# Kernel tuning notes

Measured on AMD Instinct MI355X. Metric: run time of the kernel, lower is better.

Reference implementation:

```python
import jax, jax.numpy as jnp
import numpy as np

H = 64  # hidden_dimension
F = 8   # number_of_input_features
P = 64  # prediction_length
B = 1024
T = 512


def _lstm_cell(x, h, c, Wih, Whh, bih, bhh):
    # PyTorch gate order: input, forget, cell(g), output
    gates = x @ Wih.T + h @ Whh.T + (bih + bhh)  # [B, 4H]
    i, f, g, o = jnp.split(gates, 4, axis=-1)
    c_new = jax.nn.sigmoid(f) * c + jax.nn.sigmoid(i) * jnp.tanh(g)
    h_new = jax.nn.sigmoid(o) * jnp.tanh(c_new)
    return h_new, c_new


def setup_inputs() -> dict:
    key = jax.random.key(0)
    ks = jax.random.split(key, 11)
    s = 1.0 / np.sqrt(H)
    u = lambda k, shape: jax.random.uniform(k, shape, jnp.float32, -s, s)
    return {
        "input_sequence": jax.random.normal(ks[0], (B, T, F), jnp.float32),
        "enc_Wih": u(ks[1], (4 * H, F)),
        "enc_Whh": u(ks[2], (4 * H, H)),
        "enc_bih": u(ks[3], (4 * H,)),
        "enc_bhh": u(ks[4], (4 * H,)),
        "dec_Wih": u(ks[5], (4 * H, F)),
        "dec_Whh": u(ks[6], (4 * H, H)),
        "dec_bih": u(ks[7], (4 * H,)),
        "dec_bhh": u(ks[8], (4 * H,)),
        "fc_W": u(ks[9], (F, H)),
        "fc_b": u(ks[10], (F,)),
    }


def reference(input_sequence, enc_Wih, enc_Whh, enc_bih, enc_bhh,
              dec_Wih, dec_Whh, dec_bih, dec_bhh, fc_W, fc_b):
    Bn = input_sequence.shape[0]
    h0 = jnp.zeros((Bn, H), input_sequence.dtype)
    c0 = jnp.zeros((Bn, H), input_sequence.dtype)

    # ---- Encoder: scan over time ----
    xs = jnp.swapaxes(input_sequence, 0, 1)  # [T, B, F]

    def enc_step(carry, x_t):
        h, c = carry
        h, c = _lstm_cell(x_t, h, c, enc_Wih, enc_Whh, enc_bih, enc_bhh)
        return (h, c), None

    (h, c), _ = jax.lax.scan(enc_step, (h0, c0), xs)

    x_last = input_sequence[:, -1, :]  # [B, F]

    def dec_step(carry, _):
        h, c, x = carry
        h, c = _lstm_cell(x, h, c, dec_Wih, dec_Whh, dec_bih, dec_bhh)
        pred = h @ fc_W.T + fc_b  # [B, F]
        return (h, c, pred), pred

    _, preds = jax.lax.scan(dec_step, (h, c, x_last), None, length=P)
    return jnp.swapaxes(preds, 0, 1)  # [B, P, F]
```

## Files before the change

### kernel.cpp

```cpp
#include <hip/hip_runtime.h>


#define Hh 64
#define Ff 8
#define Tt 512
#define Pp 64
#define BATCH 1024
#define MB 4
#define NBLK (BATCH / MB)
#define ROWS 72
#define ABUF (16 * ROWS + 64)
#define XSTRIDE 32

typedef __attribute__((ext_vector_type(8))) _Float16 half8;
typedef __attribute__((ext_vector_type(4))) _Float16 half4;
typedef __attribute__((ext_vector_type(4))) float f32x4;

#define LOG2E  1.44269504088896340736f
#define K2LOG2 2.88538008177792681472f

__device__ __forceinline__ float sig_pre(float a) {
    return __builtin_amdgcn_rcpf(1.f + __builtin_amdgcn_exp2f(-a));
}
__device__ __forceinline__ float tanh_pre(float a) {
    return 1.f - 2.f * __builtin_amdgcn_rcpf(1.f + __builtin_amdgcn_exp2f(a));
}
__device__ __forceinline__ int arow_base(int m) { return m * ROWS + (m & 3) * 16; }

__device__ __forceinline__ void load_wfrags(
    const float* __restrict__ Whh, const float* __restrict__ Wih,
    int wv, int q, int col, half8 w0[4], half8 w1[4], half8 wx[4])
{
    #pragma unroll
    for (int Tg = 0; Tg < 4; ++Tg) {
        int g = Tg * 64 + wv * 16 + col;
        float sc = (Tg == 2) ? K2LOG2 : LOG2E;
        const float* r0 = Whh + g * 64 + q * 8;
        #pragma unroll
        for (int j = 0; j < 8; ++j) {
            w0[Tg][j] = (_Float16)(r0[j] * sc);
            w1[Tg][j] = (_Float16)(r0[32 + j] * sc);
            wx[Tg][j] = (q == 0) ? (_Float16)(Wih[g * 8 + j] * sc) : (_Float16)0.f;
        }
    }
}

__device__ __forceinline__ void pchain(half8 ax, const half8 wx[4],
                                       const f32x4 biasv[4], f32x4 P[4])
{
    P[2] = __builtin_amdgcn_mfma_f32_16x16x32_f16(ax, wx[2], biasv[2], 0, 0, 0);
    P[0] = __builtin_amdgcn_mfma_f32_16x16x32_f16(ax, wx[0], biasv[0], 0, 0, 0);
    P[1] = __builtin_amdgcn_mfma_f32_16x16x32_f16(ax, wx[1], biasv[1], 0, 0, 0);
    P[3] = __builtin_amdgcn_mfma_f32_16x16x32_f16(ax, wx[3], biasv[3], 0, 0, 0);
}

__device__ __forceinline__ float qcell(half8 a0, half8 a1,
    const half8 w0[4], const half8 w1[4], const f32x4 P[4], float& cS)
{
    f32x4 Qg = __builtin_amdgcn_mfma_f32_16x16x32_f16(a0, w0[2], P[2], 0, 0, 0);
    f32x4 Qi = __builtin_amdgcn_mfma_f32_16x16x32_f16(a0, w0[0], P[0], 0, 0, 0);
    f32x4 Qf = __builtin_amdgcn_mfma_f32_16x16x32_f16(a0, w0[1], P[1], 0, 0, 0);
    f32x4 Qo = __builtin_amdgcn_mfma_f32_16x16x32_f16(a0, w0[3], P[3], 0, 0, 0);
    Qg = __builtin_amdgcn_mfma_f32_16x16x32_f16(a1, w1[2], Qg, 0, 0, 0);
    Qi = __builtin_amdgcn_mfma_f32_16x16x32_f16(a1, w1[0], Qi, 0, 0, 0);
    Qf = __builtin_amdgcn_mfma_f32_16x16x32_f16(a1, w1[1], Qf, 0, 0, 0);
    Qo = __builtin_amdgcn_mfma_f32_16x16x32_f16(a1, w1[3], Qo, 0, 0, 0);
    float tg = tanh_pre(Qg[0]);
    float si = sig_pre(Qi[0]);
    float sf = sig_pre(Qf[0]);
    float so = sig_pre(Qo[0]);
    cS = sf * cS + (si * tg) * K2LOG2;
    return so * tanh_pre(cS);
}

__global__ __launch_bounds__(256, 1)
void seq2seq_v8(const float* __restrict__ x_seq,
                const float* __restrict__ eWih, const float* __restrict__ eWhh,
                const float* __restrict__ ebih, const float* __restrict__ ebhh,
                const float* __restrict__ dWih, const float* __restrict__ dWhh,
                const float* __restrict__ dbih, const float* __restrict__ dbhh,
                const float* __restrict__ fcW,  const float* __restrict__ fcb,
                float* __restrict__ out)
{
    __shared__ __align__(16) _Float16 xs[(Tt + 4) * XSTRIDE];
    __shared__ __align__(16) _Float16 A0[ABUF];
    __shared__ __align__(16) _Float16 A1[ABUF];
    __shared__ float fcWT[Hh * 9 + 8];
    __shared__ float sfcb[Ff];
    __shared__ __align__(16) _Float16 xdec[MB * Ff];

    const int tid  = threadIdx.x;
    const int wv   = tid >> 6;
    const int lane = tid & 63;
    const int q    = lane >> 4;
    const int col  = lane & 15;
    const int u    = wv * 16 + col;
    const int b0   = blockIdx.x * MB;

    half8 w0[4], w1[4], wx[4];
    load_wfrags(eWhh, eWih, wv, q, col, w0, w1, wx);
    f32x4 biasv[4];
    #pragma unroll
    for (int Tg = 0; Tg < 4; ++Tg) {
        int g = Tg * 64 + u;
        float sc = (Tg == 2) ? K2LOG2 : LOG2E;
        float bv = (ebih[g] + ebhh[g]) * sc;
        biasv[Tg] = (f32x4){bv, bv, bv, bv};
    }

    { int* Z0 = (int*)A0; int* Z1 = (int*)A1;
      for (int i = tid; i < ABUF / 2; i += 256) { Z0[i] = 0; Z1[i] = 0; } }
    for (int i = tid; i < Ff * Hh; i += 256) { int f = i >> 6, uu = i & 63; fcWT[uu * 9 + f] = fcW[i]; }
    if (tid < Ff) sfcb[tid] = fcb[tid];
    if (tid < 64) ((int*)xs)[Tt * 16 + tid] = 0;
    for (int i = tid; i < MB * Tt * 2; i += 256) {
        int b   = i >> 10;
        int rem = i & 1023;
        int t   = rem >> 1;
        int f4  = (rem & 1) * 4;
        const float* src = x_seq + ((size_t)(b0 + b) * Tt + t) * Ff + f4;
        half4 s = { (_Float16)src[0], (_Float16)src[1], (_Float16)src[2], (_Float16)src[3] };
        *(half4*)(&xs[t * XSTRIDE + b * 8 + f4]) = s;
    }
    __syncthreads();

    const _Float16* arA = A0 + arow_base(col) + q * 8;
    const _Float16* arB = A1 + arow_base(col) + q * 8;
    _Float16* hwA = A0 + 4 * q * ROWS + u;
    _Float16* hwB = A1 + 4 * q * ROWS + u;
    const _Float16* xq = xs + (col >> 2) * 8;

    float cS = 0.f;
    f32x4 Pc[4], Pn[4];
    half8 xa;
    {   half8 x0 = *(const half8*)(xq);
        pchain(x0, wx, biasv, Pc);
        xa = *(const half8*)(xq + XSTRIDE);
        xq += 2 * XSTRIDE; }

    for (int t = 0; t < Tt; t += 2) {
        __syncthreads();
        {
            half8 a0 = *(const half8*)(arA);
            half8 a1 = *(const half8*)(arA + 32);
            pchain(xa, wx, biasv, Pn);
            half8 xn = *(const half8*)(xq); xq += XSTRIDE;
            float hn = qcell(a0, a1, w0, w1, Pc, cS);
            *hwB = (_Float16)hn;
            xa = xn;
        }
        __syncthreads();
        {
            half8 a0 = *(const half8*)(arB);
            half8 a1 = *(const half8*)(arB + 32);
            pchain(xa, wx, biasv, Pc);
            half8 xn = *(const half8*)(xq); xq += XSTRIDE;
            float hn = qcell(a0, a1, w0, w1, Pn, cS);
            *hwA = (_Float16)hn;
            xa = xn;
        }
    }

    load_wfrags(dWhh, dWih, wv, q, col, w0, w1, wx);
    #pragma unroll
    for (int Tg = 0; Tg < 4; ++Tg) {
        int g = Tg * 64 + u;
        float sc = (Tg == 2) ? K2LOG2 : LOG2E;
        float bv = (dbih[g] + dbhh[g]) * sc;
        biasv[Tg] = (f32x4){bv, bv, bv, bv};
    }
    if (tid < MB * Ff) xdec[tid] = xs[(Tt - 1) * XSTRIDE + tid];
    __syncthreads();

    float* predbuf = (float*)xs;
    const _Float16* xdp = xdec + (col >> 2) * 8;

    for (int p = 0; p < Pp; ++p) {
        const _Float16* ar = (p & 1) ? arB : arA;
        _Float16*       hw = (p & 1) ? hwA : hwB;
        const _Float16* hb = (p & 1) ? A0  : A1;
        half8 a0 = *(const half8*)(ar);
        half8 a1 = *(const half8*)(ar + 32);
        half8 ax = *(const half8*)(xdp);
        pchain(ax, wx, biasv, Pc);
        float hn = qcell(a0, a1, w0, w1, Pc, cS);
        *hw = (_Float16)hn;
        __syncthreads();
        if (tid < MB * Ff) {
            int b = tid >> 3, f = tid & 7;
            const _Float16* hr = hb + (4 * b) * ROWS;
            float s = sfcb[f];
            #pragma unroll
            for (int ch = 0; ch < 8; ++ch) {
                half8 hh = *(const half8*)(hr + ch * 8);
                #pragma unroll
                for (int j = 0; j < 8; ++j)
                    s += (float)hh[j] * fcWT[(ch * 8 + j) * 9 + f];
            }
            predbuf[b * (Pp * Ff) + p * Ff + f] = s;
            xdec[tid] = (_Float16)s;
        }
        __syncthreads();
    }

    {
        f32x4* out4 = (f32x4*)out + (size_t)b0 * (Pp * Ff / 4);
        const f32x4* pb4 = (const f32x4*)predbuf;
        for (int i = tid; i < MB * Pp * Ff / 4; i += 256)
            out4[i] = pb4[i];
    }
}

extern "C" void kernel_launch(void* const* d_in, const int* in_sizes, int n_in,
                              void* d_out, int out_size, void* d_ws, size_t ws_size,
                              hipStream_t stream) {
    (void)in_sizes; (void)n_in; (void)d_ws; (void)ws_size; (void)out_size;
    hipLaunchKernelGGL(seq2seq_v8, dim3(NBLK), dim3(256), 0, stream,
                       (const float*)d_in[0],
                       (const float*)d_in[1], (const float*)d_in[2],
                       (const float*)d_in[3], (const float*)d_in[4],
                       (const float*)d_in[5], (const float*)d_in[6],
                       (const float*)d_in[7], (const float*)d_in[8],
                       (const float*)d_in[9], (const float*)d_in[10],
                       (float*)d_out);
}
```

Before: 261.9 us.

## Batch input projection over four timesteps per MFMA and fold gate scaling into FMAs

The encoder's input-projection MFMAs now compute four timesteps at once. The MFMA rows are reused so that each output row holds one timestep, and a shufflevector broadcasts the needed row into the recurrent accumulator. This removes most of the per-step input-projection MFMAs, and the loop is unrolled by eight steps with the x loads staggered. The activation math is also rearranged so the tanh scaling constants fold into fused multiply-adds, trimming a few VALU ops on the serial critical path. In exchange the loop body and register use grow, the xs buffer needs extra padding, and the broadcast adds lane moves.

Measured after the change: 271.0 us. 1.03x slower.

```diff
diff --git a/kernel.cpp b/kernel.cpp
--- a/kernel.cpp
+++ b/kernel.cpp
@@ -19,12 +19,8 @@
 #define LOG2E  1.44269504088896340736f
 #define K2LOG2 2.88538008177792681472f
 
-__device__ __forceinline__ float sig_pre(float a) {
-    return __builtin_amdgcn_rcpf(1.f + __builtin_amdgcn_exp2f(-a));
-}
-__device__ __forceinline__ float tanh_pre(float a) {
-    return 1.f - 2.f * __builtin_amdgcn_rcpf(1.f + __builtin_amdgcn_exp2f(a));
-}
+__device__ __forceinline__ float rcp_(float x)  { return __builtin_amdgcn_rcpf(x); }
+__device__ __forceinline__ float exp2_(float x) { return __builtin_amdgcn_exp2f(x); }
 __device__ __forceinline__ int arow_base(int m) { return m * ROWS + (m & 3) * 16; }
 
 __device__ __forceinline__ void load_wfrags(
@@ -45,36 +41,51 @@
     }
 }
 
-__device__ __forceinline__ void pchain(half8 ax, const half8 wx[4],
-                                       const f32x4 biasv[4], f32x4 P[4])
-{
-    P[2] = __builtin_amdgcn_mfma_f32_16x16x32_f16(ax, wx[2], biasv[2], 0, 0, 0);
-    P[0] = __builtin_amdgcn_mfma_f32_16x16x32_f16(ax, wx[0], biasv[0], 0, 0, 0);
-    P[1] = __builtin_amdgcn_mfma_f32_16x16x32_f16(ax, wx[1], biasv[1], 0, 0, 0);
-    P[3] = __builtin_amdgcn_mfma_f32_16x16x32_f16(ax, wx[3], biasv[3], 0, 0, 0);
+__device__ __forceinline__ void pgroup(half8 axg, const half8 wx[4],
+                                       const f32x4 biasv[4], f32x4 Pw[4])
+{
+    Pw[2] = __builtin_amdgcn_mfma_f32_16x16x32_f16(axg, wx[2], biasv[2], 0, 0, 0);
+    Pw[0] = __builtin_amdgcn_mfma_f32_16x16x32_f16(axg, wx[0], biasv[0], 0, 0, 0);
+    Pw[1] = __builtin_amdgcn_mfma_f32_16x16x32_f16(axg, wx[1], biasv[1], 0, 0, 0);
+    Pw[3] = __builtin_amdgcn_mfma_f32_16x16x32_f16(axg, wx[3], biasv[3], 0, 0, 0);
 }
 
 __device__ __forceinline__ float qcell(half8 a0, half8 a1,
-    const half8 w0[4], const half8 w1[4], const f32x4 P[4], float& cS)
-{
-    f32x4 Qg = __builtin_amdgcn_mfma_f32_16x16x32_f16(a0, w0[2], P[2], 0, 0, 0);
-    f32x4 Qi = __builtin_amdgcn_mfma_f32_16x16x32_f16(a0, w0[0], P[0], 0, 0, 0);
-    f32x4 Qf = __builtin_amdgcn_mfma_f32_16x16x32_f16(a0, w0[1], P[1], 0, 0, 0);
-    f32x4 Qo = __builtin_amdgcn_mfma_f32_16x16x32_f16(a0, w0[3], P[3], 0, 0, 0);
+    const half8 w0[4], const half8 w1[4],
+    f32x4 Cg, f32x4 Ci, f32x4 Cf, f32x4 Co, float& cS)
+{
+    f32x4 Qg = __builtin_amdgcn_mfma_f32_16x16x32_f16(a0, w0[2], Cg, 0, 0, 0);
+    f32x4 Qi = __builtin_amdgcn_mfma_f32_16x16x32_f16(a0, w0[0], Ci, 0, 0, 0);
+    f32x4 Qf = __builtin_amdgcn_mfma_f32_16x16x32_f16(a0, w0[1], Cf, 0, 0, 0);
+    f32x4 Qo = __builtin_amdgcn_mfma_f32_16x16x32_f16(a0, w0[3], Co, 0, 0, 0);
     Qg = __builtin_amdgcn_mfma_f32_16x16x32_f16(a1, w1[2], Qg, 0, 0, 0);
     Qi = __builtin_amdgcn_mfma_f32_16x16x32_f16(a1, w1[0], Qi, 0, 0, 0);
     Qf = __builtin_amdgcn_mfma_f32_16x16x32_f16(a1, w1[1], Qf, 0, 0, 0);
     Qo = __builtin_amdgcn_mfma_f32_16x16x32_f16(a1, w1[3], Qo, 0, 0, 0);
-    float tg = tanh_pre(Qg[0]);
-    float si = sig_pre(Qi[0]);
-    float sf = sig_pre(Qf[0]);
-    float so = sig_pre(Qo[0]);
-    cS = sf * cS + (si * tg) * K2LOG2;
-    return so * tanh_pre(cS);
-}
+    float rg  = rcp_(1.f + exp2_(Qg[0]));
+    float tg2 = __builtin_fmaf(rg, -2.f * K2LOG2, K2LOG2);
+    float si  = rcp_(1.f + exp2_(-Qi[0]));
+    float sf  = rcp_(1.f + exp2_(-Qf[0]));
+    float so  = rcp_(1.f + exp2_(-Qo[0]));
+    cS = __builtin_fmaf(sf, cS, si * tg2);
+    float rc = rcp_(1.f + exp2_(cS));
+    return __builtin_fmaf(rc, -2.f * so, so);
+}
+
+#define QSTEP(RD, WR, PW, R)                                                    \
+    {                                                                           \
+        half8 a0 = *(const half8*)(RD);                                         \
+        half8 a1 = *(const half8*)(RD + 32);                                    \
+        float hn = qcell(a0, a1, w0, w1,                                        \
+            __builtin_shufflevector(PW[2], PW[2], R, R, R, R),                  \
+            __builtin_shufflevector(PW[0], PW[0], R, R, R, R),                  \
+            __builtin_shufflevector(PW[1], PW[1], R, R, R, R),                  \
+            __builtin_shufflevector(PW[3], PW[3], R, R, R, R), cS);             \
+        *(WR) = (_Float16)hn;                                                   \
+    }
 
 __global__ __launch_bounds__(256, 1)
-void seq2seq_v8(const float* __restrict__ x_seq,
+void seq2seq_v9(const float* __restrict__ x_seq,
                 const float* __restrict__ eWih, const float* __restrict__ eWhh,
                 const float* __restrict__ ebih, const float* __restrict__ ebhh,
                 const float* __restrict__ dWih, const float* __restrict__ dWhh,
@@ -82,7 +93,7 @@
                 const float* __restrict__ fcW,  const float* __restrict__ fcb,
                 float* __restrict__ out)
 {
-    __shared__ __align__(16) _Float16 xs[(Tt + 4) * XSTRIDE];
+    __shared__ __align__(16) _Float16 xs[(Tt + 8) * XSTRIDE];
     __shared__ __align__(16) _Float16 A0[ABUF];
     __shared__ __align__(16) _Float16 A1[ABUF];
     __shared__ float fcWT[Hh * 9 + 8];
@@ -112,7 +123,7 @@
       for (int i = tid; i < ABUF / 2; i += 256) { Z0[i] = 0; Z1[i] = 0; } }
     for (int i = tid; i < Ff * Hh; i += 256) { int f = i >> 6, uu = i & 63; fcWT[uu * 9 + f] = fcW[i]; }
     if (tid < Ff) sfcb[tid] = fcb[tid];
-    if (tid < 64) ((int*)xs)[Tt * 16 + tid] = 0;
+    if (tid < 128) ((int*)xs)[Tt * 16 + tid] = 0;
     for (int i = tid; i < MB * Tt * 2; i += 256) {
         int b   = i >> 10;
         int rem = i & 1023;
@@ -128,37 +139,29 @@
     const _Float16* arB = A1 + arow_base(col) + q * 8;
     _Float16* hwA = A0 + 4 * q * ROWS + u;
     _Float16* hwB = A1 + 4 * q * ROWS + u;
-    const _Float16* xq = xs + (col >> 2) * 8;
+    const _Float16* xgp = xs + (col & 3) * XSTRIDE + (col >> 2) * 8;
 
     float cS = 0.f;
-    f32x4 Pc[4], Pn[4];
-    half8 xa;
-    {   half8 x0 = *(const half8*)(xq);
-        pchain(x0, wx, biasv, Pc);
-        xa = *(const half8*)(xq + XSTRIDE);
-        xq += 2 * XSTRIDE; }
-
-    for (int t = 0; t < Tt; t += 2) {
-        __syncthreads();
-        {
-            half8 a0 = *(const half8*)(arA);
-            half8 a1 = *(const half8*)(arA + 32);
-            pchain(xa, wx, biasv, Pn);
-            half8 xn = *(const half8*)(xq); xq += XSTRIDE;
-            float hn = qcell(a0, a1, w0, w1, Pc, cS);
-            *hwB = (_Float16)hn;
-            xa = xn;
-        }
-        __syncthreads();
-        {
-            half8 a0 = *(const half8*)(arB);
-            half8 a1 = *(const half8*)(arB + 32);
-            pchain(xa, wx, biasv, Pc);
-            half8 xn = *(const half8*)(xq); xq += XSTRIDE;
-            float hn = qcell(a0, a1, w0, w1, Pn, cS);
-            *hwA = (_Float16)hn;
-            xa = xn;
-        }
+    f32x4 PwA[4], PwB[4];
+    half8 axA, axB;
+    {   half8 ax0 = *(const half8*)(xgp); xgp += 4 * XSTRIDE;
+        pgroup(ax0, wx, biasv, PwA);
+        axB = *(const half8*)(xgp); xgp += 4 * XSTRIDE;
+    }
+
+    for (int it = 0; it < Tt / 8; ++it) {
+        __syncthreads(); QSTEP(arA, hwB, PwA, 0);
+        __syncthreads(); QSTEP(arB, hwA, PwA, 1);
+        __syncthreads(); pgroup(axB, wx, biasv, PwB);
+                         QSTEP(arA, hwB, PwA, 2);
+        __syncthreads(); axA = *(const half8*)(xgp); xgp += 4 * XSTRIDE;
+                         QSTEP(arB, hwA, PwA, 3);
+        __syncthreads(); QSTEP(arA, hwB, PwB, 0);
+        __syncthreads(); QSTEP(arB, hwA, PwB, 1);
+        __syncthreads(); pgroup(axA, wx, biasv, PwA);
+                         QSTEP(arA, hwB, PwB, 2);
+        __syncthreads(); axB = *(const half8*)(xgp); xgp += 4 * XSTRIDE;
+                         QSTEP(arB, hwA, PwB, 3);
     }
 
     load_wfrags(dWhh, dWih, wv, q, col, w0, w1, wx);
@@ -179,11 +182,11 @@
         const _Float16* ar = (p & 1) ? arB : arA;
         _Float16*       hw = (p & 1) ? hwA : hwB;
         const _Float16* hb = (p & 1) ? A0  : A1;
+        half8 ax = *(const half8*)(xdp);
+        pgroup(ax, wx, biasv, PwA);
         half8 a0 = *(const half8*)(ar);
         half8 a1 = *(const half8*)(ar + 32);
-        half8 ax = *(const half8*)(xdp);
-        pchain(ax, wx, biasv, Pc);
-        float hn = qcell(a0, a1, w0, w1, Pc, cS);
+        float hn = qcell(a0, a1, w0, w1, PwA[2], PwA[0], PwA[1], PwA[3], cS);
         *hw = (_Float16)hn;
         __syncthreads();
         if (tid < MB * Ff) {
@@ -215,7 +218,7 @@
                               void* d_out, int out_size, void* d_ws, size_t ws_size,
                               hipStream_t stream) {
     (void)in_sizes; (void)n_in; (void)d_ws; (void)ws_size; (void)out_size;
-    hipLaunchKernelGGL(seq2seq_v8, dim3(NBLK), dim3(256), 0, stream,
+    hipLaunchKernelGGL(seq2seq_v9, dim3(NBLK), dim3(256), 0, stream,
                        (const float*)d_in[0],
                        (const float*)d_in[1], (const float*)d_in[2],
                        (const float*)d_in[3], (const float*)d_in[4],
```
